# Performance work log

Measured on AMD Instinct MI355X. Metric: run time of the kernel, lower is better.

Reference implementation:

```python
import jax, jax.numpy as jnp
import numpy as np

N_NODES = 100000
N_EDGES = 3200000
IN_CH = 128
HID = 8
HEADS = 8
NEG_SLOPE = 0.2  # PyG GATConv default


def setup_inputs() -> dict:
    key = jax.random.key(0)
    ks = jax.random.split(key, 12)
    s = 0.1
    return {
        "x": jax.random.normal(ks[0], (N_NODES, IN_CH), jnp.float32),
        "edge_index": jax.random.randint(ks[1], (2, N_EDGES), 0, N_NODES, dtype=jnp.int64),
        "W1": jax.random.normal(ks[2], (IN_CH, HEADS * HID), jnp.float32) * s,
        "a_src1": jax.random.normal(ks[3], (1, HEADS, HID), jnp.float32) * s,
        "a_dst1": jax.random.normal(ks[4], (1, HEADS, HID), jnp.float32) * s,
        "b1": jax.random.normal(ks[5], (HEADS * HID,), jnp.float32) * s,
        "W2": jax.random.normal(ks[6], (HEADS * HID, HID), jnp.float32) * s,
        "a_src2": jax.random.normal(ks[7], (1, 1, HID), jnp.float32) * s,
        "a_dst2": jax.random.normal(ks[8], (1, 1, HID), jnp.float32) * s,
        "b2": jax.random.normal(ks[9], (HID,), jnp.float32) * s,
        "Wc": jax.random.normal(ks[10], (HID, 2), jnp.float32) * s,
        "bc": jax.random.normal(ks[11], (2,), jnp.float32) * s,
    }


def gat_conv(x, src, dst, W, a_src, a_dst, b, concat):
    """PyG-style GATConv (eval mode, self-loops already appended to src/dst)."""
    n = x.shape[0]
    H, C = a_src.shape[1], a_src.shape[2]
    h = (x @ W).reshape(n, H, C)                       # [N,H,C]
    alpha_src = jnp.sum(h * a_src, axis=-1)            # [N,H]
    alpha_dst = jnp.sum(h * a_dst, axis=-1)            # [N,H]
    e = jax.nn.leaky_relu(alpha_src[src] + alpha_dst[dst], NEG_SLOPE)  # [E,H]
    # segment softmax over destination-node neighborhoods
    m = jax.ops.segment_max(e, dst, num_segments=n)    # [N,H]
    m = jnp.where(jnp.isfinite(m), m, 0.0)
    p = jnp.exp(e - m[dst])
    z = jax.ops.segment_sum(p, dst, num_segments=n)    # [N,H]
    alpha = p / (z[dst] + 1e-16)                       # [E,H]
    out = jax.ops.segment_sum(alpha[..., None] * h[src], dst, num_segments=n)  # [N,H,C]
    out = out.reshape(n, H * C) if concat else out.mean(axis=1)
    return out + b


def reference(x, edge_index, W1, a_src1, a_dst1, b1, W2, a_src2, a_dst2, b2, Wc, bc):
    n = x.shape[0]
    loops = jnp.arange(n, dtype=edge_index.dtype)
    src = jnp.concatenate([edge_index[0], loops])
    dst = jnp.concatenate([edge_index[1], loops])
    h = jax.nn.relu(gat_conv(x, src, dst, W1, a_src1, a_dst1, b1, concat=True))
    embeddings = gat_conv(h, src, dst, W2, a_src2, a_dst2, b2, concat=False)
    logits = embeddings @ Wc + bc
    return embeddings, logits
```

## Files before the change

kernel.cpp:

```cpp
#include <hip/hip_runtime.h>
#include <hip/hip_bf16.h>

#define NN 100000
#define IN_CH 128
#define HID 8
#define HEADS 8
#define HC 64
#define BSH 8
#define NBUCK ((NN + 255) >> 8)
#define NBLK 512
#define PCAP 10240
#define LOG2E 1.44269504088896340736f

__device__ __forceinline__ unsigned short f2bf(float f) {
    unsigned u = __float_as_uint(f);
    unsigned r = (u + 0x7fffu + ((u >> 16) & 1u)) >> 16;
    return (unsigned short)r;
}


__global__ __launch_bounds__(256) void k_bincount(const int* __restrict__ ei, int E, int ET,
                                                  int cpb, int* __restrict__ cnt) {
    __shared__ int h[NBUCK];
    for (int i = threadIdx.x; i < NBUCK; i += 256) h[i] = 0;
    __syncthreads();
    int beg = blockIdx.x * cpb, end = min(ET, beg + cpb);
    for (int t = beg + threadIdx.x; t < end; t += 256) {
        int d = (t < E) ? ei[E + t] : (t - E);
        atomicAdd(&h[d >> BSH], 1);
    }
    __syncthreads();
    for (int i = threadIdx.x; i < NBUCK; i += 256) cnt[i * NBLK + blockIdx.x] = h[i];
}

__global__ __launch_bounds__(256) void k_colscan(int* __restrict__ cnt, int* __restrict__ btot) {
    __shared__ int sd[256];
    int t = threadIdx.x;
    int* col = cnt + blockIdx.x * NBLK;
    int v0 = col[2 * t], v1 = col[2 * t + 1];
    int s = v0 + v1;
    sd[t] = s;
    __syncthreads();
    for (int off = 1; off < 256; off <<= 1) {
        int u = (t >= off) ? sd[t - off] : 0;
        __syncthreads();
        sd[t] += u;
        __syncthreads();
    }
    int excl = sd[t] - s;
    col[2 * t] = excl;
    col[2 * t + 1] = excl + v0;
    if (t == 255) btot[blockIdx.x] = excl + s;
}

__global__ __launch_bounds__(256) void k_bucketbase(const int* __restrict__ btot,
                                                    int* __restrict__ bbase,
                                                    int* __restrict__ row_ptr) {
    __shared__ int sd[256];
    int t = threadIdx.x;
    int v0 = (2 * t < NBUCK) ? btot[2 * t] : 0;
    int v1 = (2 * t + 1 < NBUCK) ? btot[2 * t + 1] : 0;
    int s = v0 + v1;
    sd[t] = s;
    __syncthreads();
    for (int off = 1; off < 256; off <<= 1) {
        int u = (t >= off) ? sd[t - off] : 0;
        __syncthreads();
        sd[t] += u;
        __syncthreads();
    }
    int excl = sd[t] - s;
    if (2 * t < NBUCK) bbase[2 * t] = excl;
    if (2 * t + 1 < NBUCK) bbase[2 * t + 1] = excl + v0;
    if (t == 255) { bbase[NBUCK] = excl + s; row_ptr[NN] = excl + s; }
}

__global__ __launch_bounds__(256) void k_binscatter(const int* __restrict__ ei, int E, int ET,
                                                    int cpb, const int* __restrict__ cnt,
                                                    const int* __restrict__ bbase,
                                                    unsigned* __restrict__ pairs) {
    __shared__ int cur[NBUCK];
    for (int i = threadIdx.x; i < NBUCK; i += 256)
        cur[i] = bbase[i] + cnt[i * NBLK + blockIdx.x];
    __syncthreads();
    int beg = blockIdx.x * cpb, end = min(ET, beg + cpb);
    for (int t = beg + threadIdx.x; t < end; t += 256) {
        int s, d;
        if (t < E) { s = ei[t]; d = ei[E + t]; } else { s = t - E; d = t - E; }
        int pos = atomicAdd(&cur[d >> BSH], 1);
        pairs[pos] = ((unsigned)s << 8) | (unsigned)(d & 255);
    }
}

__global__ __launch_bounds__(256) void k_bucketscatter(const unsigned* __restrict__ pairs,
                                                       const int* __restrict__ bbase,
                                                       int* __restrict__ row_ptr,
                                                       int* __restrict__ csr) {
    __shared__ unsigned pl[PCAP];
    __shared__ int h[256];
    __shared__ int sd[256];
    int b = blockIdx.x;
    int t = threadIdx.x;
    int beg = bbase[b], end = bbase[b + 1];
    int cntE = end - beg;
    bool inl = cntE <= PCAP;
    if (inl)
        for (int j = t; j < cntE; j += 256) pl[j] = pairs[beg + j];
    h[t] = 0;
    __syncthreads();
    for (int j = t; j < cntE; j += 256) {
        unsigned pv = inl ? pl[j] : pairs[beg + j];
        atomicAdd(&h[pv & 255u], 1);
    }
    __syncthreads();
    int v = h[t];
    sd[t] = v;
    __syncthreads();
    for (int off = 1; off < 256; off <<= 1) {
        int u = (t >= off) ? sd[t - off] : 0;
        __syncthreads();
        sd[t] += u;
        __syncthreads();
    }
    int excl = sd[t] - v;
    int node = (b << 8) + t;
    if (node < NN) row_ptr[node] = beg + excl;
    __syncthreads();
    h[t] = beg + excl;
    __syncthreads();
    for (int j = t; j < cntE; j += 256) {
        unsigned pv = inl ? pl[j] : pairs[beg + j];
        int pos = atomicAdd(&h[pv & 255u], 1);
        csr[pos] = (int)(pv >> 8);
    }
}


__global__ __launch_bounds__(256) void k_gemm1(const float* __restrict__ x,
                                               const float* __restrict__ W1,
                                               const float* __restrict__ aS,
                                               const float* __restrict__ aD,
                                               unsigned* __restrict__ h1q,
                                               float* __restrict__ scale1,
                                               float* __restrict__ asrc1,
                                               float* __restrict__ adst1) {
    __shared__ float wl[IN_CH * HC];
    int tid = threadIdx.x;
    {
        const float4* Wg4 = (const float4*)W1;
        float4* wl4 = (float4*)wl;
#pragma unroll
        for (int i = 0; i < 8; ++i) wl4[tid + i * 256] = Wg4[tid + i * 256];
    }
    __syncthreads();
    int lane = tid & 63;
    int row = blockIdx.x * 16 + (tid >> 6) * 4 + (lane >> 4);
    int c0 = (lane & 15) * 4;
    const float4* xr = (const float4*)(x + (size_t)row * IN_CH);
    float4 acc = make_float4(0.f, 0.f, 0.f, 0.f);
#pragma unroll 4
    for (int kq = 0; kq < IN_CH / 4; ++kq) {
        float4 xv = xr[kq];
        const float4* wrow = (const float4*)(wl + (kq * 4) * HC + c0);
        float4 w0 = wrow[0];
        float4 w1 = wrow[HC / 4];
        float4 w2 = wrow[2 * (HC / 4)];
        float4 w3 = wrow[3 * (HC / 4)];
        acc.x += xv.x * w0.x + xv.y * w1.x + xv.z * w2.x + xv.w * w3.x;
        acc.y += xv.x * w0.y + xv.y * w1.y + xv.z * w2.y + xv.w * w3.y;
        acc.z += xv.x * w0.z + xv.y * w1.z + xv.z * w2.z + xv.w * w3.z;
        acc.w += xv.x * w0.w + xv.y * w1.w + xv.z * w2.w + xv.w * w3.w;
    }
    float am = fmaxf(fmaxf(fabsf(acc.x), fabsf(acc.y)), fmaxf(fabsf(acc.z), fabsf(acc.w)));
    am = fmaxf(am, __shfl_xor(am, 1, 64));
    am = fmaxf(am, __shfl_xor(am, 2, 64));
    am = fmaxf(am, __shfl_xor(am, 4, 64));
    am = fmaxf(am, __shfl_xor(am, 8, 64));
    am = fmaxf(am, 1e-20f);
    float qinv = 127.0f / am;
    int q0 = __float2int_rn(acc.x * qinv);
    int q1 = __float2int_rn(acc.y * qinv);
    int q2 = __float2int_rn(acc.z * qinv);
    int q3 = __float2int_rn(acc.w * qinv);
    unsigned u = (unsigned)(q0 & 255) | ((unsigned)(q1 & 255) << 8) |
                 ((unsigned)(q2 & 255) << 16) | ((unsigned)(q3 & 255) << 24);
    h1q[row * 16 + (lane & 15)] = u;
    if ((lane & 15) == 0) scale1[row] = am * (1.0f / 127.0f);
    int head = (lane & 15) >> 1;
    int cl = c0 & 7;
    const float* as = aS + head * 8 + cl;
    const float* ad = aD + head * 8 + cl;
    float ps = acc.x * as[0] + acc.y * as[1] + acc.z * as[2] + acc.w * as[3];
    float pd = acc.x * ad[0] + acc.y * ad[1] + acc.z * ad[2] + acc.w * ad[3];
    ps += __shfl_xor(ps, 1, 64);
    pd += __shfl_xor(pd, 1, 64);
    if ((lane & 1) == 0) {
        asrc1[row * 8 + head] = ps * LOG2E;
        adst1[row * 8 + head] = pd * LOG2E;
    }
}


__global__ __launch_bounds__(256) void k_agg1(const int* __restrict__ row_ptr,
                                              const int* __restrict__ csr,
                                              const float* __restrict__ asrc1,
                                              const float* __restrict__ adst1,
                                              const uint2* __restrict__ h1q,
                                              const float* __restrict__ scale1,
                                              const float* __restrict__ b1,
                                              const float* __restrict__ W2,
                                              const float* __restrict__ aS2,
                                              const float* __restrict__ aD2,
                                              unsigned short* __restrict__ h2bf,
                                              float* __restrict__ asrc2,
                                              float* __restrict__ adst2) {
    int tid = threadIdx.x;
    int lane = tid & 63;
    int slot = lane >> 3;
    int hl = lane & 7;
    float w2r[8];
#pragma unroll
    for (int i = 0; i < 8; ++i) w2r[i] = W2[(hl * 8 + i) * 8 + slot];
    float4 b0 = *(const float4*)(b1 + hl * 8);
    float4 b1v = *(const float4*)(b1 + hl * 8 + 4);
    float as2 = aS2[slot], ad2 = aD2[slot];
    int nbase = (blockIdx.x * 4 + (tid >> 6)) * 4;
    for (int ni = 0; ni < 4; ++ni) {
        int n = nbase + ni;
        float adst = adst1[n * 8 + hl];
        int beg = row_ptr[n], end = row_ptr[n + 1];
        int nit = (end - beg + 7) >> 3;
        float z = 0.f;
        float4 accA = make_float4(0.f, 0.f, 0.f, 0.f);
        float4 accB = make_float4(0.f, 0.f, 0.f, 0.f);
        int j0 = beg + slot;
        bool v0 = j0 < end;
        int s0 = v0 ? csr[j0] : 0;
        int j1 = j0 + 8;
        bool v1 = j1 < end;
        int s1 = v1 ? csr[j1] : 0;
        float a0 = asrc1[(size_t)s0 * 8 + hl];
        float c0 = scale1[s0];
        uint2 r0 = h1q[(size_t)s0 * 8 + hl];
        int jn = j1;
        for (int it = 0; it < nit; ++it) {
            int j2 = jn + 8;
            bool v2 = j2 < end;
            int s2 = v2 ? csr[j2] : 0;
            float a1 = asrc1[(size_t)s1 * 8 + hl];
            float c1 = scale1[s1];
            uint2 r1 = h1q[(size_t)s1 * 8 + hl];
            float e = a0 + adst;
            e = fmaxf(e, 0.2f * e);
            float p = v0 ? exp2f(e) : 0.f;
            float ps = p * c0;
            z += p;
            accA.x += ps * (float)(((int)(r0.x << 24)) >> 24);
            accA.y += ps * (float)(((int)(r0.x << 16)) >> 24);
            accA.z += ps * (float)(((int)(r0.x << 8)) >> 24);
            accA.w += ps * (float)(((int)r0.x) >> 24);
            accB.x += ps * (float)(((int)(r0.y << 24)) >> 24);
            accB.y += ps * (float)(((int)(r0.y << 16)) >> 24);
            accB.z += ps * (float)(((int)(r0.y << 8)) >> 24);
            accB.w += ps * (float)(((int)r0.y) >> 24);
            v0 = v1; a0 = a1; c0 = c1; r0 = r1;
            v1 = v2; s1 = s2;
            jn = j2;
        }
#pragma unroll
        for (int off = 8; off <= 32; off <<= 1) {
            z += __shfl_xor(z, off, 64);
            accA.x += __shfl_xor(accA.x, off, 64);
            accA.y += __shfl_xor(accA.y, off, 64);
            accA.z += __shfl_xor(accA.z, off, 64);
            accA.w += __shfl_xor(accA.w, off, 64);
            accB.x += __shfl_xor(accB.x, off, 64);
            accB.y += __shfl_xor(accB.y, off, 64);
            accB.z += __shfl_xor(accB.z, off, 64);
            accB.w += __shfl_xor(accB.w, off, 64);
        }
        float inv = 1.f / (z + 1e-16f);
        float hr0 = fmaxf(accA.x * inv + b0.x, 0.f);
        float hr1 = fmaxf(accA.y * inv + b0.y, 0.f);
        float hr2 = fmaxf(accA.z * inv + b0.z, 0.f);
        float hr3 = fmaxf(accA.w * inv + b0.w, 0.f);
        float hr4 = fmaxf(accB.x * inv + b1v.x, 0.f);
        float hr5 = fmaxf(accB.y * inv + b1v.y, 0.f);
        float hr6 = fmaxf(accB.z * inv + b1v.z, 0.f);
        float hr7 = fmaxf(accB.w * inv + b1v.w, 0.f);
        float part = hr0 * w2r[0] + hr1 * w2r[1] + hr2 * w2r[2] + hr3 * w2r[3] +
                     hr4 * w2r[4] + hr5 * w2r[5] + hr6 * w2r[6] + hr7 * w2r[7];
        part += __shfl_xor(part, 1, 64);
        part += __shfl_xor(part, 2, 64);
        part += __shfl_xor(part, 4, 64);
        if (hl == 0) {
            h2bf[(size_t)n * 8 + slot] = f2bf(part);
            float s2v = part * as2;
            float d2v = part * ad2;
            s2v += __shfl_xor(s2v, 8, 64);
            s2v += __shfl_xor(s2v, 16, 64);
            s2v += __shfl_xor(s2v, 32, 64);
            d2v += __shfl_xor(d2v, 8, 64);
            d2v += __shfl_xor(d2v, 16, 64);
            d2v += __shfl_xor(d2v, 32, 64);
            if (slot == 0) {
                asrc2[n] = s2v * LOG2E;
                adst2[n] = d2v * LOG2E;
            }
        }
    }
}


__global__ __launch_bounds__(256) void k_agg2(const int* __restrict__ row_ptr,
                                              const int* __restrict__ csr,
                                              const float* __restrict__ asrc2,
                                              const float* __restrict__ adst2,
                                              const unsigned short* __restrict__ h2bf,
                                              const float* __restrict__ b2,
                                              const float* __restrict__ Wc,
                                              const float* __restrict__ bc,
                                              float* __restrict__ out) {
    int tid = threadIdx.x;
    int lane = tid & 63;
    int n = blockIdx.x * 4 + (tid >> 6);
    int slot = lane >> 3;
    int sl = lane & 7;
    float adst = adst2[n];
    int beg = row_ptr[n], end = row_ptr[n + 1];
    int nit = (end - beg + 7) >> 3;
    float z = 0.f, acc = 0.f;
    int j0 = beg + slot;
    bool v0 = j0 < end;
    int s0 = v0 ? csr[j0] : 0;
    int j1 = j0 + 8;
    bool v1 = j1 < end;
    int s1 = v1 ? csr[j1] : 0;
    float a0 = asrc2[s0];
    unsigned short u0 = h2bf[(size_t)s0 * 8 + sl];
    int jn = j1;
    for (int it = 0; it < nit; ++it) {
        int j2 = jn + 8;
        bool v2 = j2 < end;
        int s2 = v2 ? csr[j2] : 0;
        float a1 = asrc2[s1];
        unsigned short u1 = h2bf[(size_t)s1 * 8 + sl];
        float e = a0 + adst;
        e = fmaxf(e, 0.2f * e);
        float p = v0 ? exp2f(e) : 0.f;
        float h0 = __uint_as_float(((unsigned)u0) << 16);
        z += p;
        acc += p * h0;
        v0 = v1; a0 = a1; u0 = u1;
        v1 = v2; s1 = s2;
        jn = j2;
    }
#pragma unroll
    for (int off = 8; off <= 32; off <<= 1) {
        z += __shfl_xor(z, off, 64);
        acc += __shfl_xor(acc, off, 64);
    }
    float emb = acc / (z + 1e-16f) + b2[sl];
    if (slot == 0) out[(size_t)n * HID + sl] = emb;
    float t0 = emb * Wc[sl * 2 + 0];
    float t1 = emb * Wc[sl * 2 + 1];
    t0 += __shfl_xor(t0, 1, 64); t0 += __shfl_xor(t0, 2, 64); t0 += __shfl_xor(t0, 4, 64);
    t1 += __shfl_xor(t1, 1, 64); t1 += __shfl_xor(t1, 2, 64); t1 += __shfl_xor(t1, 4, 64);
    if (lane == 0) {
        out[(size_t)NN * HID + n * 2 + 0] = t0 + bc[0];
        out[(size_t)NN * HID + n * 2 + 1] = t1 + bc[1];
    }
}


extern "C" void kernel_launch(void* const* d_in, const int* in_sizes, int n_in,
                              void* d_out, int out_size, void* d_ws, size_t ws_size,
                              hipStream_t stream) {
    const float* x  = (const float*)d_in[0];
    const int*   ei = (const int*)d_in[1];
    const float* W1 = (const float*)d_in[2];
    const float* aS = (const float*)d_in[3];
    const float* aD = (const float*)d_in[4];
    const float* b1 = (const float*)d_in[5];
    const float* W2 = (const float*)d_in[6];
    const float* aS2 = (const float*)d_in[7];
    const float* aD2 = (const float*)d_in[8];
    const float* b2 = (const float*)d_in[9];
    const float* Wc = (const float*)d_in[10];
    const float* bc = (const float*)d_in[11];

    int E = in_sizes[1] / 2;
    int N = NN;
    int ET = E + N;
    int cpb = (ET + NBLK - 1) / NBLK;

    char* p = (char*)d_ws;
    auto alloc = [&](size_t bytes) -> char* {
        char* r = p;
        p += (bytes + 255) & ~(size_t)255;
        return r;
    };
    unsigned* h1q   = (unsigned*)alloc((size_t)N * 16 * 4);
    float* scale1   = (float*)alloc((size_t)N * 4);
    float* asrc1    = (float*)alloc((size_t)N * 8 * 4);
    float* adst1    = (float*)alloc((size_t)N * 8 * 4);
    unsigned short* h2bf = (unsigned short*)alloc((size_t)N * 8 * 2);
    float* asrc2    = (float*)alloc((size_t)N * 4);
    float* adst2    = (float*)alloc((size_t)N * 4);
    int*   row_ptr  = (int*)alloc((size_t)(N + 1) * 4);
    int*   cnt      = (int*)alloc((size_t)NBUCK * NBLK * 4);
    int*   btot     = (int*)alloc((size_t)NBUCK * 4);
    int*   bbase    = (int*)alloc((size_t)(NBUCK + 1) * 4);
    int*   csr      = (int*)alloc((size_t)ET * 4);
    unsigned* pairs = (unsigned*)alloc((size_t)ET * 4);

    k_bincount<<<NBLK, 256, 0, stream>>>(ei, E, ET, cpb, cnt);
    k_colscan<<<NBUCK, 256, 0, stream>>>(cnt, btot);
    k_bucketbase<<<1, 256, 0, stream>>>(btot, bbase, row_ptr);
    k_binscatter<<<NBLK, 256, 0, stream>>>(ei, E, ET, cpb, cnt, bbase, pairs);
    k_bucketscatter<<<NBUCK, 256, 0, stream>>>(pairs, bbase, row_ptr, csr);

    k_gemm1<<<N / 16, 256, 0, stream>>>(x, W1, aS, aD, h1q, scale1, asrc1, adst1);
    k_agg1<<<N / 16, 256, 0, stream>>>(row_ptr, csr, asrc1, adst1, (const uint2*)h1q,
                                       scale1, b1, W2, aS2, aD2, h2bf, asrc2, adst2);
    k_agg2<<<N / 4, 256, 0, stream>>>(row_ptr, csr, asrc2, adst2, h2bf, b2, Wc, bc,
                                      (float*)d_out);
}
```

Measured before the change: 245.6 us.

## Split layer-1 aggregation into two head-half passes with compact half-major features

Layer-1 features and source attention logits are rearranged into two head-half planes, and aggregation runs as two passes, each gathering only half the heads. This shrinks each pass's random-gather working set so it fits the cache better. Int8 values are stored with a +128 offset and corrected after accumulation, and source logits are stored as fp16. CSR buckets shrink from 256 to 128 nodes, and the bucket-base scan handles 4 entries per thread. The cost is an extra launch, a second read of the CSR, and a partial-sum buffer written and read between passes.

```diff
diff --git a/kernel.cpp b/kernel.cpp
--- a/kernel.cpp
+++ b/kernel.cpp
@@ -1,15 +1,16 @@
 #include <hip/hip_runtime.h>
 #include <hip/hip_bf16.h>
+#include <hip/hip_fp16.h>
 
 #define NN 100000
 #define IN_CH 128
 #define HID 8
 #define HEADS 8
 #define HC 64
-#define BSH 8
-#define NBUCK ((NN + 255) >> 8)
+#define BSH 7
+#define NBUCK ((NN + 127) >> 7)
 #define NBLK 512
-#define PCAP 10240
+#define PCAP 8192
 #define LOG2E 1.44269504088896340736f
 
 __device__ __forceinline__ unsigned short f2bf(float f) {
@@ -58,9 +59,14 @@
                                                     int* __restrict__ row_ptr) {
     __shared__ int sd[256];
     int t = threadIdx.x;
-    int v0 = (2 * t < NBUCK) ? btot[2 * t] : 0;
-    int v1 = (2 * t + 1 < NBUCK) ? btot[2 * t + 1] : 0;
-    int s = v0 + v1;
+    int v[4];
+    int s = 0;
+#pragma unroll
+    for (int i = 0; i < 4; ++i) {
+        int gi = t * 4 + i;
+        v[i] = (gi < NBUCK) ? btot[gi] : 0;
+        s += v[i];
+    }
     sd[t] = s;
     __syncthreads();
     for (int off = 1; off < 256; off <<= 1) {
@@ -70,9 +76,13 @@
         __syncthreads();
     }
     int excl = sd[t] - s;
-    if (2 * t < NBUCK) bbase[2 * t] = excl;
-    if (2 * t + 1 < NBUCK) bbase[2 * t + 1] = excl + v0;
-    if (t == 255) { bbase[NBUCK] = excl + s; row_ptr[NN] = excl + s; }
+#pragma unroll
+    for (int i = 0; i < 4; ++i) {
+        int gi = t * 4 + i;
+        if (gi < NBUCK) bbase[gi] = excl;
+        excl += v[i];
+    }
+    if (t == 255) { bbase[NBUCK] = excl; row_ptr[NN] = excl; }
 }
 
 __global__ __launch_bounds__(256) void k_binscatter(const int* __restrict__ ei, int E, int ET,
@@ -88,7 +98,7 @@
         int s, d;
         if (t < E) { s = ei[t]; d = ei[E + t]; } else { s = t - E; d = t - E; }
         int pos = atomicAdd(&cur[d >> BSH], 1);
-        pairs[pos] = ((unsigned)s << 8) | (unsigned)(d & 255);
+        pairs[pos] = ((unsigned)s << 7) | (unsigned)(d & 127);
     }
 }
 
@@ -97,8 +107,8 @@
                                                        int* __restrict__ row_ptr,
                                                        int* __restrict__ csr) {
     __shared__ unsigned pl[PCAP];
-    __shared__ int h[256];
-    __shared__ int sd[256];
+    __shared__ int h[128];
+    __shared__ int sd[128];
     int b = blockIdx.x;
     int t = threadIdx.x;
     int beg = bbase[b], end = bbase[b + 1];
@@ -106,32 +116,34 @@
     bool inl = cntE <= PCAP;
     if (inl)
         for (int j = t; j < cntE; j += 256) pl[j] = pairs[beg + j];
-    h[t] = 0;
+    if (t < 128) h[t] = 0;
     __syncthreads();
     for (int j = t; j < cntE; j += 256) {
         unsigned pv = inl ? pl[j] : pairs[beg + j];
-        atomicAdd(&h[pv & 255u], 1);
-    }
-    __syncthreads();
-    int v = h[t];
-    sd[t] = v;
-    __syncthreads();
-    for (int off = 1; off < 256; off <<= 1) {
-        int u = (t >= off) ? sd[t - off] : 0;
-        __syncthreads();
-        sd[t] += u;
-        __syncthreads();
-    }
-    int excl = sd[t] - v;
-    int node = (b << 8) + t;
-    if (node < NN) row_ptr[node] = beg + excl;
-    __syncthreads();
-    h[t] = beg + excl;
+        atomicAdd(&h[pv & 127u], 1);
+    }
+    __syncthreads();
+    int v = 0;
+    if (t < 128) { v = h[t]; sd[t] = v; }
+    __syncthreads();
+    for (int off = 1; off < 128; off <<= 1) {
+        int u = 0;
+        if (t < 128 && t >= off) u = sd[t - off];
+        __syncthreads();
+        if (t < 128) sd[t] += u;
+        __syncthreads();
+    }
+    if (t < 128) {
+        int excl = sd[t] - v;
+        int node = (b << 7) + t;
+        if (node < NN) row_ptr[node] = beg + excl;
+        h[t] = beg + excl;
+    }
     __syncthreads();
     for (int j = t; j < cntE; j += 256) {
         unsigned pv = inl ? pl[j] : pairs[beg + j];
-        int pos = atomicAdd(&h[pv & 255u], 1);
-        csr[pos] = (int)(pv >> 8);
+        int pos = atomicAdd(&h[pv & 127u], 1);
+        csr[pos] = (int)(pv >> 7);
     }
 }
 
@@ -140,10 +152,10 @@
                                                const float* __restrict__ W1,
                                                const float* __restrict__ aS,
                                                const float* __restrict__ aD,
-                                               unsigned* __restrict__ h1q,
-                                               float* __restrict__ scale1,
-                                               float* __restrict__ asrc1,
-                                               float* __restrict__ adst1) {
+                                               uint2* __restrict__ h1q,
+                                               unsigned short* __restrict__ asrc1h,
+                                               float* __restrict__ adst1,
+                                               float* __restrict__ scale1) {
     __shared__ float wl[IN_CH * HC];
     int tid = threadIdx.x;
     {
@@ -178,59 +190,66 @@
     am = fmaxf(am, __shfl_xor(am, 8, 64));
     am = fmaxf(am, 1e-20f);
     float qinv = 127.0f / am;
-    int q0 = __float2int_rn(acc.x * qinv);
-    int q1 = __float2int_rn(acc.y * qinv);
-    int q2 = __float2int_rn(acc.z * qinv);
-    int q3 = __float2int_rn(acc.w * qinv);
-    unsigned u = (unsigned)(q0 & 255) | ((unsigned)(q1 & 255) << 8) |
-                 ((unsigned)(q2 & 255) << 16) | ((unsigned)(q3 & 255) << 24);
-    h1q[row * 16 + (lane & 15)] = u;
-    if ((lane & 15) == 0) scale1[row] = am * (1.0f / 127.0f);
-    int head = (lane & 15) >> 1;
+    int q0 = __float2int_rn(acc.x * qinv) + 128;
+    int q1 = __float2int_rn(acc.y * qinv) + 128;
+    int q2 = __float2int_rn(acc.z * qinv) + 128;
+    int q3 = __float2int_rn(acc.w * qinv) + 128;
+    unsigned u = (unsigned)q0 | ((unsigned)q1 << 8) | ((unsigned)q2 << 16) | ((unsigned)q3 << 24);
+    unsigned upart = __shfl_xor(u, 1, 64);
+    int hd = (lane & 15) >> 1;
+    int half = hd >> 2, hin = hd & 3;
     int cl = c0 & 7;
-    const float* as = aS + head * 8 + cl;
-    const float* ad = aD + head * 8 + cl;
+    const float* as = aS + hd * 8 + cl;
+    const float* ad = aD + hd * 8 + cl;
     float ps = acc.x * as[0] + acc.y * as[1] + acc.z * as[2] + acc.w * as[3];
     float pd = acc.x * ad[0] + acc.y * ad[1] + acc.z * ad[2] + acc.w * ad[3];
     ps += __shfl_xor(ps, 1, 64);
     pd += __shfl_xor(pd, 1, 64);
     if ((lane & 1) == 0) {
-        asrc1[row * 8 + head] = ps * LOG2E;
-        adst1[row * 8 + head] = pd * LOG2E;
-    }
-}
-
-
-__global__ __launch_bounds__(256) void k_agg1(const int* __restrict__ row_ptr,
-                                              const int* __restrict__ csr,
-                                              const float* __restrict__ asrc1,
-                                              const float* __restrict__ adst1,
-                                              const uint2* __restrict__ h1q,
-                                              const float* __restrict__ scale1,
-                                              const float* __restrict__ b1,
-                                              const float* __restrict__ W2,
-                                              const float* __restrict__ aS2,
-                                              const float* __restrict__ aD2,
-                                              unsigned short* __restrict__ h2bf,
-                                              float* __restrict__ asrc2,
-                                              float* __restrict__ adst2) {
+        h1q[((size_t)half * NN + row) * 4 + hin] = make_uint2(u, upart);
+        asrc1h[((size_t)half * NN + row) * 4 + hin] =
+            __half_as_ushort(__float2half(ps * LOG2E));
+        adst1[row * 8 + hd] = pd * LOG2E;
+    }
+    if ((lane & 15) == 0) scale1[row] = am * (1.0f / 127.0f);
+}
+
+
+__global__ __launch_bounds__(256) void k_agg1pass(int half,
+                                                  const int* __restrict__ row_ptr,
+                                                  const int* __restrict__ csr,
+                                                  const unsigned short* __restrict__ asrc1h,
+                                                  const float* __restrict__ adst1,
+                                                  const uint2* __restrict__ h1q,
+                                                  const float* __restrict__ scale1,
+                                                  const float* __restrict__ b1,
+                                                  const float* __restrict__ W2,
+                                                  const float* __restrict__ aS2,
+                                                  const float* __restrict__ aD2,
+                                                  float* __restrict__ h2p,
+                                                  unsigned short* __restrict__ h2bf,
+                                                  float* __restrict__ asrc2,
+                                                  float* __restrict__ adst2) {
     int tid = threadIdx.x;
     int lane = tid & 63;
-    int slot = lane >> 3;
-    int hl = lane & 7;
+    int local = lane & 31;
+    int slot = local >> 2;
+    int hd = local & 3;
     float w2r[8];
 #pragma unroll
-    for (int i = 0; i < 8; ++i) w2r[i] = W2[(hl * 8 + i) * 8 + slot];
-    float4 b0 = *(const float4*)(b1 + hl * 8);
-    float4 b1v = *(const float4*)(b1 + hl * 8 + 4);
+    for (int i = 0; i < 8; ++i) w2r[i] = W2[((half * 4 + hd) * 8 + i) * 8 + slot];
+    const float4* bp = (const float4*)(b1 + (half * 4 + hd) * 8);
+    float4 br0 = bp[0], br1 = bp[1];
     float as2 = aS2[slot], ad2 = aD2[slot];
-    int nbase = (blockIdx.x * 4 + (tid >> 6)) * 4;
+    const uint2* hq = h1q + (size_t)half * NN * 4;
+    const unsigned short* ah = asrc1h + (size_t)half * NN * 4;
+    int nbase = (blockIdx.x * 4 + (tid >> 6)) * 8 + (lane >> 5);
     for (int ni = 0; ni < 4; ++ni) {
-        int n = nbase + ni;
-        float adst = adst1[n * 8 + hl];
+        int n = nbase + ni * 2;
+        float adst = adst1[n * 8 + half * 4 + hd];
         int beg = row_ptr[n], end = row_ptr[n + 1];
         int nit = (end - beg + 7) >> 3;
-        float z = 0.f;
+        float z = 0.f, zs = 0.f;
         float4 accA = make_float4(0.f, 0.f, 0.f, 0.f);
         float4 accB = make_float4(0.f, 0.f, 0.f, 0.f);
         int j0 = beg + slot;
@@ -239,37 +258,39 @@
         int j1 = j0 + 8;
         bool v1 = j1 < end;
         int s1 = v1 ? csr[j1] : 0;
-        float a0 = asrc1[(size_t)s0 * 8 + hl];
-        float c0 = scale1[s0];
-        uint2 r0 = h1q[(size_t)s0 * 8 + hl];
+        unsigned short a0 = ah[(size_t)s0 * 4 + hd];
+        float c0s = scale1[s0];
+        uint2 r0 = hq[(size_t)s0 * 4 + hd];
         int jn = j1;
         for (int it = 0; it < nit; ++it) {
             int j2 = jn + 8;
             bool v2 = j2 < end;
             int s2 = v2 ? csr[j2] : 0;
-            float a1 = asrc1[(size_t)s1 * 8 + hl];
-            float c1 = scale1[s1];
-            uint2 r1 = h1q[(size_t)s1 * 8 + hl];
-            float e = a0 + adst;
+            unsigned short a1 = ah[(size_t)s1 * 4 + hd];
+            float c1s = scale1[s1];
+            uint2 r1 = hq[(size_t)s1 * 4 + hd];
+            float e = __half2float(__ushort_as_half(a0)) + adst;
             e = fmaxf(e, 0.2f * e);
             float p = v0 ? exp2f(e) : 0.f;
-            float ps = p * c0;
+            float ps = p * c0s;
             z += p;
-            accA.x += ps * (float)(((int)(r0.x << 24)) >> 24);
-            accA.y += ps * (float)(((int)(r0.x << 16)) >> 24);
-            accA.z += ps * (float)(((int)(r0.x << 8)) >> 24);
-            accA.w += ps * (float)(((int)r0.x) >> 24);
-            accB.x += ps * (float)(((int)(r0.y << 24)) >> 24);
-            accB.y += ps * (float)(((int)(r0.y << 16)) >> 24);
-            accB.z += ps * (float)(((int)(r0.y << 8)) >> 24);
-            accB.w += ps * (float)(((int)r0.y) >> 24);
-            v0 = v1; a0 = a1; c0 = c1; r0 = r1;
+            zs += ps;
+            accA.x += ps * (float)(r0.x & 255u);
+            accA.y += ps * (float)((r0.x >> 8) & 255u);
+            accA.z += ps * (float)((r0.x >> 16) & 255u);
+            accA.w += ps * (float)(r0.x >> 24);
+            accB.x += ps * (float)(r0.y & 255u);
+            accB.y += ps * (float)((r0.y >> 8) & 255u);
+            accB.z += ps * (float)((r0.y >> 16) & 255u);
+            accB.w += ps * (float)(r0.y >> 24);
+            v0 = v1; a0 = a1; c0s = c1s; r0 = r1;
             v1 = v2; s1 = s2;
             jn = j2;
         }
 #pragma unroll
-        for (int off = 8; off <= 32; off <<= 1) {
+        for (int off = 4; off <= 16; off <<= 1) {
             z += __shfl_xor(z, off, 64);
+            zs += __shfl_xor(zs, off, 64);
             accA.x += __shfl_xor(accA.x, off, 64);
             accA.y += __shfl_xor(accA.y, off, 64);
             accA.z += __shfl_xor(accA.z, off, 64);
@@ -280,32 +301,37 @@
             accB.w += __shfl_xor(accB.w, off, 64);
         }
         float inv = 1.f / (z + 1e-16f);
-        float hr0 = fmaxf(accA.x * inv + b0.x, 0.f);
-        float hr1 = fmaxf(accA.y * inv + b0.y, 0.f);
-        float hr2 = fmaxf(accA.z * inv + b0.z, 0.f);
-        float hr3 = fmaxf(accA.w * inv + b0.w, 0.f);
-        float hr4 = fmaxf(accB.x * inv + b1v.x, 0.f);
-        float hr5 = fmaxf(accB.y * inv + b1v.y, 0.f);
-        float hr6 = fmaxf(accB.z * inv + b1v.z, 0.f);
-        float hr7 = fmaxf(accB.w * inv + b1v.w, 0.f);
+        float zc = 128.f * zs;
+        float hr0 = fmaxf((accA.x - zc) * inv + br0.x, 0.f);
+        float hr1 = fmaxf((accA.y - zc) * inv + br0.y, 0.f);
+        float hr2 = fmaxf((accA.z - zc) * inv + br0.z, 0.f);
+        float hr3 = fmaxf((accA.w - zc) * inv + br0.w, 0.f);
+        float hr4 = fmaxf((accB.x - zc) * inv + br1.x, 0.f);
+        float hr5 = fmaxf((accB.y - zc) * inv + br1.y, 0.f);
+        float hr6 = fmaxf((accB.z - zc) * inv + br1.z, 0.f);
+        float hr7 = fmaxf((accB.w - zc) * inv + br1.w, 0.f);
         float part = hr0 * w2r[0] + hr1 * w2r[1] + hr2 * w2r[2] + hr3 * w2r[3] +
                      hr4 * w2r[4] + hr5 * w2r[5] + hr6 * w2r[6] + hr7 * w2r[7];
         part += __shfl_xor(part, 1, 64);
         part += __shfl_xor(part, 2, 64);
-        part += __shfl_xor(part, 4, 64);
-        if (hl == 0) {
-            h2bf[(size_t)n * 8 + slot] = f2bf(part);
-            float s2v = part * as2;
-            float d2v = part * ad2;
-            s2v += __shfl_xor(s2v, 8, 64);
-            s2v += __shfl_xor(s2v, 16, 64);
-            s2v += __shfl_xor(s2v, 32, 64);
-            d2v += __shfl_xor(d2v, 8, 64);
-            d2v += __shfl_xor(d2v, 16, 64);
-            d2v += __shfl_xor(d2v, 32, 64);
-            if (slot == 0) {
-                asrc2[n] = s2v * LOG2E;
-                adst2[n] = d2v * LOG2E;
+        if (hd == 0) {
+            if (half == 0) {
+                h2p[(size_t)n * 8 + slot] = part;
+            } else {
+                float tot = part + h2p[(size_t)n * 8 + slot];
+                h2bf[(size_t)n * 8 + slot] = f2bf(tot);
+                float s2v = tot * as2;
+                float d2v = tot * ad2;
+                s2v += __shfl_xor(s2v, 4, 64);
+                s2v += __shfl_xor(s2v, 8, 64);
+                s2v += __shfl_xor(s2v, 16, 64);
+                d2v += __shfl_xor(d2v, 4, 64);
+                d2v += __shfl_xor(d2v, 8, 64);
+                d2v += __shfl_xor(d2v, 16, 64);
+                if (local == 0) {
+                    asrc2[n] = s2v * LOG2E;
+                    adst2[n] = d2v * LOG2E;
+                }
             }
         }
     }
@@ -400,10 +426,11 @@
         p += (bytes + 255) & ~(size_t)255;
         return r;
     };
-    unsigned* h1q   = (unsigned*)alloc((size_t)N * 16 * 4);
+    uint2* h1q      = (uint2*)alloc((size_t)2 * N * 4 * 8);
+    unsigned short* asrc1h = (unsigned short*)alloc((size_t)2 * N * 4 * 2);
+    float* adst1    = (float*)alloc((size_t)N * 8 * 4);
     float* scale1   = (float*)alloc((size_t)N * 4);
-    float* asrc1    = (float*)alloc((size_t)N * 8 * 4);
-    float* adst1    = (float*)alloc((size_t)N * 8 * 4);
+    float* h2p      = (float*)alloc((size_t)N * 8 * 4);
     unsigned short* h2bf = (unsigned short*)alloc((size_t)N * 8 * 2);
     float* asrc2    = (float*)alloc((size_t)N * 4);
     float* adst2    = (float*)alloc((size_t)N * 4);
@@ -420,9 +447,11 @@
     k_binscatter<<<NBLK, 256, 0, stream>>>(ei, E, ET, cpb, cnt, bbase, pairs);
     k_bucketscatter<<<NBUCK, 256, 0, stream>>>(pairs, bbase, row_ptr, csr);
 
-    k_gemm1<<<N / 16, 256, 0, stream>>>(x, W1, aS, aD, h1q, scale1, asrc1, adst1);
-    k_agg1<<<N / 16, 256, 0, stream>>>(row_ptr, csr, asrc1, adst1, (const uint2*)h1q,
-                                       scale1, b1, W2, aS2, aD2, h2bf, asrc2, adst2);
+    k_gemm1<<<N / 16, 256, 0, stream>>>(x, W1, aS, aD, h1q, asrc1h, adst1, scale1);
+    k_agg1pass<<<N / 32, 256, 0, stream>>>(0, row_ptr, csr, asrc1h, adst1, h1q, scale1,
+                                           b1, W2, aS2, aD2, h2p, h2bf, asrc2, adst2);
+    k_agg1pass<<<N / 32, 256, 0, stream>>>(1, row_ptr, csr, asrc1h, adst1, h1q, scale1,
+                                           b1, W2, aS2, aD2, h2p, h2bf, asrc2, adst2);
     k_agg2<<<N / 4, 256, 0, stream>>>(row_ptr, csr, asrc2, adst2, h2bf, b2, Wc, bc,
                                       (float*)d_out);
 }
```

New measurement: 285.0 us. 16.0% more time.
